# Kernel tuning notes

Hardware: AMD Instinct MI355X
Metric: run time of the kernel (lower is better)

The kernel has to match this reference:

```python
import jax, jax.numpy as jnp
import numpy as np
import math

D_MODEL = 1024
NUM_HEADS = 16
HEAD_DIM = D_MODEL // NUM_HEADS
CLAMP = 1e9


def setup_inputs() -> dict:
    key = jax.random.key(0)
    k1, k2, k3, k4, k5 = jax.random.split(key, 5)
    B, S = 2, 2048
    x = jax.random.normal(k1, (B, S, D_MODEL), dtype=jnp.float32)
    # torch Linear params, stored as [in, out] (y = x @ W + b)
    s1 = 1.0 / math.sqrt(D_MODEL)
    W_qkv = jax.random.uniform(k2, (D_MODEL, 3 * D_MODEL), jnp.float32, -s1, s1)
    b_qkv = jax.random.uniform(k3, (3 * D_MODEL,), jnp.float32, -s1, s1)
    W_out = jax.random.uniform(k4, (D_MODEL, D_MODEL), jnp.float32, -s1, s1)
    b_out = jax.random.uniform(k5, (D_MODEL,), jnp.float32, -s1, s1)
    return {"x": x, "W_qkv": W_qkv, "b_qkv": b_qkv, "W_out": W_out, "b_out": b_out}


def reference(x, W_qkv, b_qkv, W_out, b_out):
    B, S, D = x.shape
    qkv = x @ W_qkv + b_qkv                       # [B, S, 3*D]
    qkv = qkv.reshape(B, S, NUM_HEADS, 3 * HEAD_DIM).transpose(0, 2, 1, 3)  # [B, H, S, 3*hd]
    q, k, v = jnp.split(qkv, 3, axis=-1)          # each [B, H, S, hd]
    scale = 1.0 / math.sqrt(HEAD_DIM)
    scores = jnp.einsum('bhqd,bhkd->bhqk', q, k) * scale  # [B, H, S, S]
    causal = jnp.tril(jnp.ones((S, S), dtype=bool))
    scores = jnp.where(causal, scores, -jnp.inf)
    scores = jnp.clip(scores, -CLAMP, CLAMP)      # -inf -> -1e9, matching torch clamp
    attn = jax.nn.softmax(scores, axis=-1)
    values = jnp.einsum('bhqk,bhkd->bhqd', attn, v)        # [B, H, S, hd]
    values = values.transpose(0, 2, 1, 3).reshape(B, S, D)  # [B, S, D]
    out = values @ W_out + b_out
    # dropout is identity in eval mode
    return out
```

## Files before the change

### kernel.cpp

```cpp
#include <hip/hip_runtime.h>
#include <hip/hip_bf16.h>

#define D_MODEL 1024
#define NUM_HEADS 16
#define HEAD_DIM 64
#define SEQ 2048
#define BATCH 2
#define ROWS (BATCH * SEQ)

typedef unsigned short u16;
typedef __bf16 bf16x8 __attribute__((ext_vector_type(8)));
typedef float f32x4 __attribute__((ext_vector_type(4)));

__device__ inline u16 f2bfu(float f) {
  unsigned u = __float_as_uint(f);
  unsigned r = (u + 0x7fffu + ((u >> 16) & 1u)) >> 16;
  return (u16)r;
}

__device__ inline unsigned cvt_pk_bf16(float a, float b) {
#if __has_builtin(__builtin_amdgcn_cvt_pk_bf16_f32)
  auto r = __builtin_amdgcn_cvt_pk_bf16_f32(a, b);
  unsigned u;
  __builtin_memcpy(&u, &r, 4);
  return u;
#else
  return (unsigned)f2bfu(a) | ((unsigned)f2bfu(b) << 16);
#endif
}

__device__ inline f32x4 mfma16(bf16x8 a, bf16x8 b, f32x4 c) {
  return __builtin_amdgcn_mfma_f32_16x16x32_bf16(a, b, c, 0, 0, 0);
}

__device__ inline bf16x8 load_frag(const u16* p) {
  union { uint4 v; bf16x8 f; } u;
  u.v = *(const uint4*)p;
  return u.f;
}

__device__ inline void gload_lds16(const u16* g, u16* l) {
  __builtin_amdgcn_global_load_lds((const __attribute__((address_space(1))) void*)g,
                                   (__attribute__((address_space(3))) void*)l, 16, 0, 0);
}


__global__ __launch_bounds__(256) void prep_kernel(const float* __restrict__ x,
                                                   u16* __restrict__ xb,
                                                   const float* __restrict__ Wq,
                                                   u16* __restrict__ WqT,
                                                   const float* __restrict__ Wo,
                                                   u16* __restrict__ WoT) {
  __shared__ float t[32][33];
  const int bid = blockIdx.x;
  if (bid < 4096) {
    int i = bid * 256 + threadIdx.x;
    float4 v = ((const float4*)x)[i];
    uint2 o;
    o.x = cvt_pk_bf16(v.x, v.y);
    o.y = cvt_pk_bf16(v.z, v.w);
    ((uint2*)xb)[i] = o;
    return;
  }
  const float* W;
  u16* Wt;
  int N, tIdx;
  if (bid < 4096 + 3072) { W = Wq; Wt = WqT; N = 3072; tIdx = bid - 4096; }
  else                   { W = Wo; Wt = WoT; N = 1024; tIdx = bid - 7168; }
  const int k0 = (tIdx & 31) * 32, n0 = (tIdx >> 5) * 32;
  const int c = threadIdx.x & 31, r8 = threadIdx.x >> 5;
#pragma unroll
  for (int i = 0; i < 4; i++) {
    int r = r8 + i * 8;
    t[r][c] = W[(size_t)(k0 + r) * N + n0 + c];
  }
  __syncthreads();
#pragma unroll
  for (int i = 0; i < 4; i++) {
    int r = r8 + i * 8;
    Wt[(size_t)(n0 + r) * 1024 + k0 + c] = f2bfu(t[c][r]);
  }
}


__global__ __launch_bounds__(256, 3) void gemm_qkv(const u16* __restrict__ A,
                                                   const u16* __restrict__ Bt,
                                                   const float* __restrict__ bias,
                                                   u16* __restrict__ Qb, u16* __restrict__ Kb,
                                                   u16* __restrict__ Vt) {
  __shared__ u16 lA0[128 * 32], lB0[128 * 32];
  __shared__ u16 lA1[128 * 32], lB1[128 * 32];
  const int tid = threadIdx.x;
  const int wave = tid >> 6, lane = tid & 63, ln = lane & 15, quad = lane >> 4;
  const int n0 = blockIdx.x * 128, m0 = blockIdx.y * 128;
  const int wm = (wave & 1) * 64, wn = (wave >> 1) * 64;
  f32x4 acc[4][4] = {};

  auto issue = [&](u16* dA, u16* dB, int k0) {
#pragma unroll
    for (int i = 0; i < 2; ++i) {
      int rb = wave * 2 + i;
      gload_lds16(A + (size_t)(m0 + rb * 16 + ln) * 1024 + k0 + quad * 8, dA + rb * 512);
      gload_lds16(Bt + (size_t)(n0 + rb * 16 + ln) * 1024 + k0 + quad * 8, dB + rb * 512);
    }
  };
  auto compute = [&](const u16* sA, const u16* sB) {
    bf16x8 a[4], b[4];
#pragma unroll
    for (int i = 0; i < 4; ++i) {
      a[i] = load_frag(sA + (wm / 16 + i) * 512 + quad * 128 + ln * 8);
      b[i] = load_frag(sB + (wn / 16 + i) * 512 + quad * 128 + ln * 8);
    }
#pragma unroll
    for (int mt = 0; mt < 4; ++mt)
#pragma unroll
      for (int nt = 0; nt < 4; ++nt) acc[mt][nt] = mfma16(a[mt], b[nt], acc[mt][nt]);
  };

  issue(lA0, lB0, 0);
  for (int p = 0; p < 15; ++p) {
    asm volatile("s_barrier" ::: "memory");
    issue(lA1, lB1, (2 * p + 1) * 32);
    asm volatile("s_waitcnt vmcnt(4)" ::: "memory");
    asm volatile("s_barrier" ::: "memory");
    compute(lA0, lB0);
    asm volatile("s_barrier" ::: "memory");
    issue(lA0, lB0, (2 * p + 2) * 32);
    asm volatile("s_waitcnt vmcnt(4)" ::: "memory");
    asm volatile("s_barrier" ::: "memory");
    compute(lA1, lB1);
  }
  asm volatile("s_barrier" ::: "memory");
  issue(lA1, lB1, 31 * 32);
  asm volatile("s_waitcnt vmcnt(4)" ::: "memory");
  asm volatile("s_barrier" ::: "memory");
  compute(lA0, lB0);
  asm volatile("s_waitcnt vmcnt(0)" ::: "memory");
  asm volatile("s_barrier" ::: "memory");
  compute(lA1, lB1);

#pragma unroll
  for (int mt = 0; mt < 4; ++mt) {
    int row = m0 + wm + mt * 16 + quad * 4;
    int bb = row >> 11, s0 = row & 2047;
#pragma unroll
    for (int nt = 0; nt < 4; ++nt) {
      int col = n0 + wn + nt * 16 + ln;
      float bv = bias[col];
      int h = col / 192, rem = col - h * 192, t3 = rem >> 6, d = rem & 63;
      int bh = bb * NUM_HEADS + h;
      if (t3 == 2) {
        uint2 pk;
        pk.x = cvt_pk_bf16(acc[mt][nt][0] + bv, acc[mt][nt][1] + bv);
        pk.y = cvt_pk_bf16(acc[mt][nt][2] + bv, acc[mt][nt][3] + bv);
        *(uint2*)(Vt + ((size_t)bh * 64 + d) * SEQ + s0) = pk;
      } else {
        u16* dst = (t3 == 0) ? Qb : Kb;
#pragma unroll
        for (int r = 0; r < 4; ++r)
          dst[((size_t)bh * SEQ + s0 + r) * 64 + d] = f2bfu(acc[mt][nt][r] + bv);
      }
    }
  }
}


__global__ __launch_bounds__(512) void attn_kernel(const u16* __restrict__ Qb,
                                                   const u16* __restrict__ Kb,
                                                   const u16* __restrict__ Vt,
                                                   u16* __restrict__ Ob) {
  __shared__ u16 lK[2 * 64 * 64];
  __shared__ u16 lV[2 * 64 * 64];
  __shared__ u16 lP[8][1152];
  const int tid = threadIdx.x;
  const int wave = tid >> 6, lane = tid & 63;
  const int ln = lane & 15, quad = lane >> 4;
  const int j = blockIdx.x;
  const int lo = j, hi = 31 - j;
  const int myt = (wave < 4) ? lo : hi;
  const int q0w = myt * 64 + (wave & 3) * 16;
  const int sD = myt >> 1;
  const int nsup = (hi + 2) >> 1;
  const int bh = blockIdx.y;
  const u16* Qg = Qb + (size_t)bh * SEQ * 64;
  const u16* Kg = Kb + (size_t)bh * SEQ * 64;
  const u16* Vg = Vt + (size_t)bh * 64 * SEQ;
  u16* lPw = lP[wave];

  bf16x8 qf[2];
#pragma unroll
  for (int ks = 0; ks < 2; ++ks)
    qf[ks] = load_frag(Qg + (size_t)(q0w + ln) * 64 + ks * 32 + quad * 8);

  const u16* sp[4];
  u16* dp[4];
  const int sstep = (wave < 4) ? 128 * 64 : 128;
#pragma unroll
  for (int i = 0; i < 4; ++i) {
    int c = wave * 4 + i;
    if (c < 16) {
      int half = c >> 3, cc = c & 7, rb = cc >> 1, kgh = cc & 1;
      sp[i] = Kg + (size_t)(half * 64 + rb * 16 + ln) * 64 + (kgh * 4 + quad) * 8;
      dp[i] = lK + half * 4096 + rb * 1024 + kgh * 512;
    } else {
      int c2 = c - 16, half = c2 >> 3, cc = c2 & 7, rb = cc >> 1, kgh = cc & 1;
      sp[i] = Vg + (size_t)(rb * 16 + ln) * SEQ + half * 64 + (kgh * 4 + quad) * 8;
      dp[i] = lV + half * 4096 + rb * 1024 + kgh * 512;
    }
  }

  f32x4 o[4] = {};
  float m_r = -1e30f;
  float l_r = 0.f;
  const float SC = 0.18033688011112042f;
  const int qq = q0w + ln;

  for (int s = 0; s < nsup; ++s) {
    __syncthreads();
#pragma unroll
    for (int i = 0; i < 4; ++i) { gload_lds16(sp[i], dp[i]); sp[i] += sstep; }
    __syncthreads();

    if (s <= sD) {
      f32x4 sc[2][4] = {};
#pragma unroll
      for (int h = 0; h < 2; ++h)
#pragma unroll
        for (int mt = 0; mt < 4; ++mt)
#pragma unroll
          for (int ks = 0; ks < 2; ++ks) {
            bf16x8 kf = load_frag(lK + h * 4096 + mt * 1024 + (ks * 4 + quad) * 128 + ln * 8);
            sc[h][mt] = mfma16(kf, qf[ks], sc[h][mt]);
          }
      if (s == sD) {
#pragma unroll
        for (int h = 0; h < 2; ++h)
#pragma unroll
          for (int mt = 0; mt < 4; ++mt) {
            int key0 = (2 * s + h) * 64 + mt * 16 + quad * 4;
#pragma unroll
            for (int r = 0; r < 4; ++r)
              if (key0 + r > qq) sc[h][mt][r] = -1e30f;
          }
      }
      float mloc = sc[0][0][0];
#pragma unroll
      for (int h = 0; h < 2; ++h)
#pragma unroll
        for (int mt = 0; mt < 4; ++mt)
#pragma unroll
          for (int r = 0; r < 4; ++r) mloc = fmaxf(mloc, sc[h][mt][r]);
      mloc = fmaxf(mloc, __shfl_xor(mloc, 16));
      mloc = fmaxf(mloc, __shfl_xor(mloc, 32));
      float mnew = fmaxf(m_r, mloc);
      float alpha = __builtin_amdgcn_exp2f((m_r - mnew) * SC);
      float nmsc = -mnew * SC;
      float sum = 0.f;
#pragma unroll
      for (int h = 0; h < 2; ++h)
#pragma unroll
        for (int mt = 0; mt < 4; ++mt)
#pragma unroll
          for (int r = 0; r < 4; ++r) {
            float p = __builtin_amdgcn_exp2f(__builtin_fmaf(sc[h][mt][r], SC, nmsc));
            sc[h][mt][r] = p;
            sum += p;
          }
      sum += __shfl_xor(sum, 16);
      sum += __shfl_xor(sum, 32);
      l_r = l_r * alpha + sum;
      m_r = mnew;
#pragma unroll
      for (int dt = 0; dt < 4; ++dt) o[dt] *= alpha;

#pragma unroll
      for (int h = 0; h < 2; ++h) {
#pragma unroll
        for (int mt = 0; mt < 4; ++mt) {
          uint2 pk;
          pk.x = cvt_pk_bf16(sc[h][mt][0], sc[h][mt][1]);
          pk.y = cvt_pk_bf16(sc[h][mt][2], sc[h][mt][3]);
          int addr = ln * 64 + (((mt * 2 + (quad >> 1)) ^ (ln & 7)) * 8) + (quad & 1) * 4;
          *(uint2*)(lPw + addr) = pk;
        }
        bf16x8 pf[2];
#pragma unroll
        for (int ks = 0; ks < 2; ++ks)
          pf[ks] = load_frag(lPw + ln * 64 + (((ks * 4 + quad) ^ (ln & 7)) * 8));
#pragma unroll
        for (int dt = 0; dt < 4; ++dt)
#pragma unroll
          for (int ks = 0; ks < 2; ++ks) {
            bf16x8 av = load_frag(lV + h * 4096 + dt * 1024 + (ks * 4 + quad) * 128 + ln * 8);
            o[dt] = mfma16(av, pf[ks], o[dt]);
          }
      }
    }
  }

  float inv = 1.f / l_r;
#pragma unroll
  for (int dt = 0; dt < 4; ++dt) {
    uint2 pk;
    pk.x = cvt_pk_bf16(o[dt][0] * inv, o[dt][1] * inv);
    pk.y = cvt_pk_bf16(o[dt][2] * inv, o[dt][3] * inv);
    *(uint2*)(lPw + ln * 72 + dt * 16 + quad * 4) = pk;
  }
  const int b = bh >> 4, h2 = bh & 15;
#pragma unroll
  for (int i = 0; i < 2; ++i) {
    int c = lane + i * 64;
    int qq2 = c >> 3, dg = c & 7;
    uint4 val = *(const uint4*)(lPw + qq2 * 72 + dg * 8);
    *(uint4*)(Ob + ((size_t)b * SEQ + q0w + qq2) * 1024 + h2 * 64 + dg * 8) = val;
  }
}


__global__ __launch_bounds__(256, 3) void gemm_out(const u16* __restrict__ A,
                                                   const u16* __restrict__ Bt,
                                                   const float* __restrict__ bias,
                                                   float* __restrict__ out) {
  __shared__ u16 lA0[128 * 32], lB0[64 * 32];
  __shared__ u16 lA1[128 * 32], lB1[64 * 32];
  const int tid = threadIdx.x;
  const int wave = tid >> 6, lane = tid & 63, ln = lane & 15, quad = lane >> 4;
  const int n0 = blockIdx.x * 64, m0 = blockIdx.y * 128;
  f32x4 acc[2][4] = {};

  auto issue = [&](u16* dA, u16* dB, int k0) {
#pragma unroll
    for (int i = 0; i < 3; ++i) {
      int c = wave * 3 + i;
      if (c < 8) {
        gload_lds16(A + (size_t)(m0 + c * 16 + ln) * 1024 + k0 + quad * 8, dA + c * 512);
      } else {
        int cc = c - 8;
        gload_lds16(Bt + (size_t)(n0 + cc * 16 + ln) * 1024 + k0 + quad * 8, dB + cc * 512);
      }
    }
  };
  auto compute = [&](const u16* sA, const u16* sB) {
    bf16x8 a[2], b[4];
#pragma unroll
    for (int i = 0; i < 2; ++i)
      a[i] = load_frag(sA + (wave * 2 + i) * 512 + quad * 128 + ln * 8);
#pragma unroll
    for (int i = 0; i < 4; ++i)
      b[i] = load_frag(sB + i * 512 + quad * 128 + ln * 8);
#pragma unroll
    for (int mt = 0; mt < 2; ++mt)
#pragma unroll
      for (int nt = 0; nt < 4; ++nt) acc[mt][nt] = mfma16(a[mt], b[nt], acc[mt][nt]);
  };

  issue(lA0, lB0, 0);
  for (int p = 0; p < 15; ++p) {
    asm volatile("s_barrier" ::: "memory");
    issue(lA1, lB1, (2 * p + 1) * 32);
    asm volatile("s_waitcnt vmcnt(3)" ::: "memory");
    asm volatile("s_barrier" ::: "memory");
    compute(lA0, lB0);
    asm volatile("s_barrier" ::: "memory");
    issue(lA0, lB0, (2 * p + 2) * 32);
    asm volatile("s_waitcnt vmcnt(3)" ::: "memory");
    asm volatile("s_barrier" ::: "memory");
    compute(lA1, lB1);
  }
  asm volatile("s_barrier" ::: "memory");
  issue(lA1, lB1, 31 * 32);
  asm volatile("s_waitcnt vmcnt(3)" ::: "memory");
  asm volatile("s_barrier" ::: "memory");
  compute(lA0, lB0);
  asm volatile("s_waitcnt vmcnt(0)" ::: "memory");
  asm volatile("s_barrier" ::: "memory");
  compute(lA1, lB1);

#pragma unroll
  for (int mt = 0; mt < 2; ++mt) {
    int row = m0 + wave * 32 + mt * 16 + quad * 4;
#pragma unroll
    for (int nt = 0; nt < 4; ++nt) {
      int col = n0 + nt * 16 + ln;
      float bv = bias[col];
#pragma unroll
      for (int r = 0; r < 4; ++r)
        out[(size_t)(row + r) * 1024 + col] = acc[mt][nt][r] + bv;
    }
  }
}


extern "C" void kernel_launch(void* const* d_in, const int* in_sizes, int n_in,
                              void* d_out, int out_size, void* d_ws, size_t ws_size,
                              hipStream_t stream) {
  const float* x = (const float*)d_in[0];
  const float* W_qkv = (const float*)d_in[1];
  const float* b_qkv = (const float*)d_in[2];
  const float* W_out = (const float*)d_in[3];
  const float* b_out = (const float*)d_in[4];
  float* out = (float*)d_out;

  char* ws = (char*)d_ws;
  const size_t SZ_XB = (size_t)ROWS * D_MODEL * 2;
  const size_t SZ_WQKVT = (size_t)3 * D_MODEL * D_MODEL * 2;
  const size_t SZ_WOUTT = (size_t)D_MODEL * D_MODEL * 2;
  const size_t SZ_HEADS = (size_t)BATCH * NUM_HEADS * SEQ * HEAD_DIM * 2;
  u16* xb = (u16*)(ws);
  u16* WqkvT = (u16*)(ws + SZ_XB);
  u16* WoutT = (u16*)(ws + SZ_XB + SZ_WQKVT);
  u16* Qb = (u16*)(ws + SZ_XB + SZ_WQKVT + SZ_WOUTT);
  u16* Kb = (u16*)(ws + SZ_XB + SZ_WQKVT + SZ_WOUTT + SZ_HEADS);
  u16* Vt = (u16*)(ws + SZ_XB + SZ_WQKVT + SZ_WOUTT + 2 * SZ_HEADS);
  u16* Ob = (u16*)(ws + SZ_XB + SZ_WQKVT + SZ_WOUTT + 3 * SZ_HEADS);

  prep_kernel<<<dim3(8192), dim3(256), 0, stream>>>(x, xb, W_qkv, WqkvT, W_out, WoutT);
  gemm_qkv<<<dim3(3 * D_MODEL / 128, ROWS / 128), dim3(256), 0, stream>>>(xb, WqkvT, b_qkv,
                                                                          Qb, Kb, Vt);
  attn_kernel<<<dim3(SEQ / 128, BATCH * NUM_HEADS), dim3(512), 0, stream>>>(Qb, Kb, Vt, Ob);
  gemm_out<<<dim3(D_MODEL / 64, ROWS / 128), dim3(256), 0, stream>>>(Ob, WoutT, b_out, out);
}
```

Before: 206.9 us.

## Rework QKV GEMM into 256x256 tiles with 4-slot LDS pipeline and swizzle

The QKV projection GEMM moves from 128x128 tiles with 256 threads and double buffering to 256x256 tiles with 512 threads. It uses a deeper multi-slot LDS ring, staging A and B halves in separate phases that are interleaved with MFMA groups. It also remaps block indices to improve L2 locality and raises wave priority around the MFMA bursts. The aim is more data reuse per loaded byte and better overlap of global loads with compute. In exchange it uses far more LDS and registers (128 KB LDS, 32 accumulators per wave), and the grid shrinks to 192 blocks, which may underfill the 256 CUs.

```diff
diff --git a/kernel.cpp b/kernel.cpp
--- a/kernel.cpp
+++ b/kernel.cpp
@@ -83,82 +83,107 @@
 }
 
 
-__global__ __launch_bounds__(256, 3) void gemm_qkv(const u16* __restrict__ A,
+__global__ __launch_bounds__(512, 2) void gemm_qkv(const u16* __restrict__ A,
                                                    const u16* __restrict__ Bt,
                                                    const float* __restrict__ bias,
                                                    u16* __restrict__ Qb, u16* __restrict__ Kb,
                                                    u16* __restrict__ Vt) {
-  __shared__ u16 lA0[128 * 32], lB0[128 * 32];
-  __shared__ u16 lA1[128 * 32], lB1[128 * 32];
+  __shared__ u16 lds[8 * 8192];
   const int tid = threadIdx.x;
   const int wave = tid >> 6, lane = tid & 63, ln = lane & 15, quad = lane >> 4;
-  const int n0 = blockIdx.x * 128, m0 = blockIdx.y * 128;
-  const int wm = (wave & 1) * 64, wn = (wave >> 1) * 64;
-  f32x4 acc[4][4] = {};
-
-  auto issue = [&](u16* dA, u16* dB, int k0) {
-#pragma unroll
-    for (int i = 0; i < 2; ++i) {
-      int rb = wave * 2 + i;
-      gload_lds16(A + (size_t)(m0 + rb * 16 + ln) * 1024 + k0 + quad * 8, dA + rb * 512);
-      gload_lds16(Bt + (size_t)(n0 + rb * 16 + ln) * 1024 + k0 + quad * 8, dB + rb * 512);
-    }
+  const int lin = blockIdx.y * 12 + blockIdx.x;
+  const int swz = (lin & 7) * 24 + (lin >> 3);
+  const int n0 = (swz % 12) * 256, m0 = (swz / 12) * 256;
+  const int wm = wave >> 2, wn = wave & 3;
+  f32x4 acc[8][4] = {};
+  bf16x8 bfr[4];
+
+  const u16* aBase = A + (size_t)(m0 + ln) * 1024 + quad * 8;
+  const u16* bBase = Bt + (size_t)(n0 + ln) * 1024 + quad * 8;
+  u16* ldsW = lds + wave * 1024;
+
+  auto stage = [&](int slot, int isB, int koff) __attribute__((always_inline)) {
+    const u16* src = (isB ? bBase : aBase) + koff;
+    u16* dst = ldsW + slot * 8192;
+    gload_lds16(src + (size_t)(wave * 2) * 16384, dst);
+    gload_lds16(src + (size_t)(wave * 2) * 16384 + 16384, dst + 512);
   };
-  auto compute = [&](const u16* sA, const u16* sB) {
-    bf16x8 a[4], b[4];
-#pragma unroll
-    for (int i = 0; i < 4; ++i) {
-      a[i] = load_frag(sA + (wm / 16 + i) * 512 + quad * 128 + ln * 8);
-      b[i] = load_frag(sB + (wn / 16 + i) * 512 + quad * 128 + ln * 8);
-    }
-#pragma unroll
-    for (int mt = 0; mt < 4; ++mt)
-#pragma unroll
-      for (int nt = 0; nt < 4; ++nt) acc[mt][nt] = mfma16(a[mt], b[nt], acc[mt][nt]);
+
+  auto do_phase = [&](int bufbase, int ph2, int stSlot, int stIsB, int stKoff,
+                      int wait) __attribute__((always_inline)) {
+    const u16* aslot = lds + (bufbase + ((ph2 & 2) ? 2 : 0)) * 8192;
+    const u16* bslot = lds + (bufbase + ((ph2 & 2) ? 3 : 1)) * 8192;
+    const int mh = ph2 & 1;
+    bf16x8 afr[4];
+#pragma unroll
+    for (int q = 0; q < 4; ++q)
+      afr[q] = load_frag(aslot + (wm * 8 + mh * 4 + q) * 512 + quad * 128 + ln * 8);
+    if (mh == 0) {
+#pragma unroll
+      for (int n = 0; n < 4; ++n)
+        bfr[n] = load_frag(bslot + (wn * 4 + n) * 512 + quad * 128 + ln * 8);
+    }
+    if (stSlot >= 0) stage(stSlot, stIsB, stKoff);
+    if (wait == 4) asm volatile("s_waitcnt vmcnt(4)" ::: "memory");
+    if (wait == 0) asm volatile("s_waitcnt vmcnt(0)" ::: "memory");
+    asm volatile("s_barrier" ::: "memory");
+    __builtin_amdgcn_s_setprio(1);
+#pragma unroll
+    for (int q = 0; q < 4; ++q)
+#pragma unroll
+      for (int n = 0; n < 4; ++n)
+        acc[mh * 4 + q][n] = mfma16(afr[q], bfr[n], acc[mh * 4 + q][n]);
+    __builtin_amdgcn_s_setprio(0);
+    asm volatile("s_barrier" ::: "memory");
   };
 
-  issue(lA0, lB0, 0);
-  for (int p = 0; p < 15; ++p) {
-    asm volatile("s_barrier" ::: "memory");
-    issue(lA1, lB1, (2 * p + 1) * 32);
-    asm volatile("s_waitcnt vmcnt(4)" ::: "memory");
-    asm volatile("s_barrier" ::: "memory");
-    compute(lA0, lB0);
-    asm volatile("s_barrier" ::: "memory");
-    issue(lA0, lB0, (2 * p + 2) * 32);
-    asm volatile("s_waitcnt vmcnt(4)" ::: "memory");
-    asm volatile("s_barrier" ::: "memory");
-    compute(lA1, lB1);
-  }
-  asm volatile("s_barrier" ::: "memory");
-  issue(lA1, lB1, 31 * 32);
+  stage(0, 0, 0);  stage(1, 1, 0);
+  stage(2, 0, 32); stage(3, 1, 32);
+  stage(4, 0, 64); stage(5, 1, 64);
   asm volatile("s_waitcnt vmcnt(4)" ::: "memory");
   asm volatile("s_barrier" ::: "memory");
-  compute(lA0, lB0);
-  asm volatile("s_waitcnt vmcnt(0)" ::: "memory");
-  asm volatile("s_barrier" ::: "memory");
-  compute(lA1, lB1);
-
-#pragma unroll
-  for (int mt = 0; mt < 4; ++mt) {
-    int row = m0 + wm + mt * 16 + quad * 4;
+
+#pragma unroll 1
+  for (int i = 0; i < 7; ++i) {
+    const int kA = 128 * i;
+    do_phase(0, 0, 6, 0, kA + 96, -1);
+    do_phase(0, 1, 7, 1, kA + 96, -1);
+    do_phase(0, 2, 0, 0, kA + 128, -1);
+    do_phase(0, 3, 1, 1, kA + 128, 4);
+    do_phase(4, 0, 2, 0, kA + 160, -1);
+    do_phase(4, 1, 3, 1, kA + 160, -1);
+    do_phase(4, 2, 4, 0, kA + 192, -1);
+    do_phase(4, 3, 5, 1, kA + 192, 4);
+  }
+  do_phase(0, 0, 6, 0, 992, -1);
+  do_phase(0, 1, 7, 1, 992, -1);
+  do_phase(0, 2, -1, 0, 0, -1);
+  do_phase(0, 3, -1, 0, 0, 0);
+  do_phase(4, 0, -1, 0, 0, -1);
+  do_phase(4, 1, -1, 0, 0, -1);
+  do_phase(4, 2, -1, 0, 0, -1);
+  do_phase(4, 3, -1, 0, 0, -1);
+
+#pragma unroll
+  for (int mf = 0; mf < 8; ++mf) {
+    int row = m0 + wm * 128 + mf * 16 + quad * 4;
     int bb = row >> 11, s0 = row & 2047;
 #pragma unroll
-    for (int nt = 0; nt < 4; ++nt) {
-      int col = n0 + wn + nt * 16 + ln;
+    for (int nf = 0; nf < 4; ++nf) {
+      int col = n0 + wn * 64 + nf * 16 + ln;
       float bv = bias[col];
       int h = col / 192, rem = col - h * 192, t3 = rem >> 6, d = rem & 63;
       int bh = bb * NUM_HEADS + h;
       if (t3 == 2) {
         uint2 pk;
-        pk.x = cvt_pk_bf16(acc[mt][nt][0] + bv, acc[mt][nt][1] + bv);
-        pk.y = cvt_pk_bf16(acc[mt][nt][2] + bv, acc[mt][nt][3] + bv);
+        pk.x = cvt_pk_bf16(acc[mf][nf][0] + bv, acc[mf][nf][1] + bv);
+        pk.y = cvt_pk_bf16(acc[mf][nf][2] + bv, acc[mf][nf][3] + bv);
         *(uint2*)(Vt + ((size_t)bh * 64 + d) * SEQ + s0) = pk;
       } else {
         u16* dst = (t3 == 0) ? Qb : Kb;
 #pragma unroll
         for (int r = 0; r < 4; ++r)
-          dst[((size_t)bh * SEQ + s0 + r) * 64 + d] = f2bfu(acc[mt][nt][r] + bv);
+          dst[((size_t)bh * SEQ + s0 + r) * 64 + d] = f2bfu(acc[mf][nf][r] + bv);
       }
     }
   }
@@ -415,7 +440,7 @@
   u16* Ob = (u16*)(ws + SZ_XB + SZ_WQKVT + SZ_WOUTT + 3 * SZ_HEADS);
 
   prep_kernel<<<dim3(8192), dim3(256), 0, stream>>>(x, xb, W_qkv, WqkvT, W_out, WoutT);
-  gemm_qkv<<<dim3(3 * D_MODEL / 128, ROWS / 128), dim3(256), 0, stream>>>(xb, WqkvT, b_qkv,
+  gemm_qkv<<<dim3(3 * D_MODEL / 256, ROWS / 256), dim3(512), 0, stream>>>(xb, WqkvT, b_qkv,
                                                                           Qb, Kb, Vt);
   attn_kernel<<<dim3(SEQ / 128, BATCH * NUM_HEADS), dim3(512), 0, stream>>>(Qb, Kb, Vt, Ob);
   gemm_out<<<dim3(D_MODEL / 64, ROWS / 128), dim3(256), 0, stream>>>(Ob, WoutT, b_out, out);
```

Result: slower. 213.1 us (+3.0%).
